# Kernel tuning notes

Hardware: AMD Instinct MI355X
Metric: run time of the kernel (lower is better)

The kernel has to match this reference:

```python
import jax, jax.numpy as jnp
import numpy as np

RU, RV = 6, 6
DU, DV = 2 * RU + 1, 2 * RV + 1  # 13, 13 displacement offsets
C = 32  # feat_channels (WipModule.c_feat)


def _conv(x, w, stride=1, pad=1):
    return jax.lax.conv_general_dilated(
        x, w, (stride, stride), [(pad, pad), (pad, pad)],
        dimension_numbers=('NCHW', 'OIHW', 'NCHW'))


def _deconv(x, w):
    # expressed as an lhs-dilated conv (kernel stored directly in OIHW conv layout).
    p = 4 - 1 - 1
    return jax.lax.conv_general_dilated(
        x, w, (1, 1), [(p, p), (p, p)], lhs_dilation=(2, 2),
        dimension_numbers=('NCHW', 'OIHW', 'NCHW'))


def _kaiming(key, shape):
    fan_in = shape[1] * shape[2] * shape[3]
    return jax.random.normal(key, shape, jnp.float32) * np.float32(np.sqrt(2.0 / fan_in))


def setup_inputs() -> dict:
    key = jax.random.key(0)
    ks = jax.random.split(key, 8)
    B, H, W = 1, 64, 128
    return {
        'fmap1': jax.random.normal(ks[0], (B, C, H, W), jnp.float32),
        'fmap2': jax.random.normal(ks[1], (B, C, H, W), jnp.float32),
        'w1': _kaiming(ks[2], (96, 2 * C, 3, 3)),
        'w2': _kaiming(ks[3], (128, 96, 3, 3)),
        'w3': _kaiming(ks[4], (128, 128, 3, 3)),
        'w4': _kaiming(ks[5], (64, 128, 3, 3)),
        'wd': _kaiming(ks[6], (32, 64, 4, 4)),
        'w5': _kaiming(ks[7], (1, 32, 3, 3)),
    }


def _build_mvol(fmap1, fmap2):
    # Vectorized form of the torch itertools.product loop: one padded gather
    # over all (du, dv) displacement windows instead of 169 slice-assignments.
    b, c, h, w = fmap1.shape
    padded = jnp.pad(fmap2, ((0, 0), (0, 0), (RV, RV), (RU, RU)))

    def window(i, j):
        # shifted(y, x) = fmap2[y + (j - RV), x + (i - RU)], zero outside bounds
        return jax.lax.dynamic_slice(padded, (0, 0, j, i), (b, c, h, w))

    shifted = jax.vmap(lambda i: jax.vmap(lambda j: window(i, j))(jnp.arange(DV)))(jnp.arange(DU))
    shifted = jnp.moveaxis(shifted, 2, 0)  # (b, du, dv, c, h, w)
    # valid mask: detached channel-sum of the warped fmap2 slice (matches torch)
    valid = (jax.lax.stop_gradient(shifted).sum(axis=3, keepdims=True) != 0)
    valid = valid.astype(fmap1.dtype)
    m1 = fmap1[:, None, None] * valid  # broadcast fmap1 over (du, dv)
    return jnp.concatenate([m1, shifted * valid], axis=3)  # (b, du, dv, 2c, h, w)


def reference(fmap1, fmap2, w1, w2, w3, w4, wd, w5):
    mvol = _build_mvol(fmap1, fmap2)
    b, du, dv, c2, h, w = mvol.shape
    # MatchingNet: fold (du, dv) into batch, conv stack down to 1 cost channel
    x = mvol.reshape(b * du * dv, c2, h, w)
    x = jax.nn.relu(_conv(x, w1))
    x = jax.nn.relu(_conv(x, w2, stride=2))  # (.., 128, h/2, w/2)
    x = jax.nn.relu(_conv(x, w3))
    x = jax.nn.relu(_conv(x, w4))
    x = jax.nn.relu(_deconv(x, wd))          # back to (h, w)
    x = _conv(x, w5)                          # cost, 1 channel
    return x.reshape(b, du, dv, h, w)
```

## Files before the change

### kernel.cpp

```cpp
#include <hip/hip_runtime.h>

#define NITEMS 169

typedef __attribute__((ext_vector_type(8))) __bf16 bf16x8;
typedef __attribute__((ext_vector_type(4))) float f32x4;
typedef __attribute__((ext_vector_type(8))) unsigned short u16x8;
typedef __attribute__((ext_vector_type(4))) unsigned short u16x4;

__device__ __forceinline__ unsigned short f2b(float x) {
  union { float f; unsigned u; } v; v.f = x;
  unsigned r = v.u + 0x7fffu + ((v.u >> 16) & 1u);
  return (unsigned short)(r >> 16);
}
__device__ __forceinline__ float b2f(unsigned short u) {
  union { unsigned u; float f; } v; v.u = ((unsigned)u) << 16;
  return v.f;
}

__global__ __launch_bounds__(256) void k_prepf(const float* __restrict__ f,
                                               unsigned short* __restrict__ fb) {
  const int pix = blockIdx.x * 256 + threadIdx.x;
  const int y = pix >> 7, x = pix & 127;
#pragma unroll
  for (int c = 0; c < 32; ++c)
    fb[(size_t)pix * 32 + c] = f2b(f[(c * 64 + y) * 128 + x]);
}

__global__ void k_prep3x3(const float* __restrict__ w, unsigned short* __restrict__ wp,
                          int Cout, int Cin) {
  int i = blockIdx.x * 256 + threadIdx.x;
  if (i >= Cout * Cin * 9) return;
  int kx = i % 3, t = i / 3;
  int ky = t % 3; t /= 3;
  int cin = t % Cin, cout = t / Cin;
  int tap = ky * 3 + kx;
  wp[(((cin >> 5) * 9 + tap) * Cout + cout) * 32 + (cin & 31)] = f2b(w[i]);
}

__global__ void k_prepwd(const float* __restrict__ w, unsigned short* __restrict__ wp) {
  int i = blockIdx.x * 256 + threadIdx.x;
  if (i >= 32 * 64 * 16) return;
  int kx = i & 3, ky = (i >> 2) & 3, ci = (i >> 4) & 63, cout = i >> 10;
  wp[(((((ci >> 5) * 4 + ky) * 4 + kx) * 32) + cout) * 32 + (ci & 31)] = f2b(w[i]);
}

__global__ __launch_bounds__(256) void k_z1(
    const unsigned short* __restrict__ f1b, const unsigned short* __restrict__ wp,
    float* __restrict__ z1) {
  const int oy0 = blockIdx.x * 2;
  constexpr int WI = 130;
  __shared__ __align__(16) unsigned short X[4][4][WI][8];
  const int wid = threadIdx.x >> 6, lane = threadIdx.x & 63;
  const int lm = lane & 15, lkg = lane >> 4, lk = lkg * 8;

  f32x4 acc[24];
#pragma unroll
  for (int t = 0; t < 24; ++t) acc[t] = f32x4{0.f, 0.f, 0.f, 0.f};

  for (int c = threadIdx.x; c < 4 * 4 * WI; c += 256) {
    const int cig = c & 3, t2 = c >> 2;
    const int col = t2 % WI, r = t2 / WI;
    const int iy = oy0 - 1 + r, ix = col - 1;
    u16x8 v = {0, 0, 0, 0, 0, 0, 0, 0};
    if ((unsigned)iy < 64u && (unsigned)ix < 128u)
      v = *(const u16x8*)&f1b[(size_t)(iy * 128 + ix) * 32 + cig * 8];
    *(u16x8*)&X[r][cig][col][0] = v;
  }
  __syncthreads();
#pragma unroll
  for (int tap = 0; tap < 9; ++tap) {
    const int ky = tap / 3, kx = tap % 3;
    bf16x8 bf[4];
#pragma unroll
    for (int j = 0; j < 4; ++j) {
      const int mt = wid * 4 + j, rw = mt >> 3, mtx = mt & 7;
      bf[j] = *(const bf16x8*)&X[rw + ky][lkg][mtx * 16 + lm + kx][0];
    }
#pragma unroll
    for (int i = 0; i < 6; ++i) {
      bf16x8 af = *(const bf16x8*)&wp[((0 * 9 + tap) * 96 + i * 16 + lm) * 32 + lk];
#pragma unroll
      for (int j = 0; j < 4; ++j)
        acc[i * 4 + j] =
            __builtin_amdgcn_mfma_f32_16x16x32_bf16(af, bf[j], acc[i * 4 + j], 0, 0, 0);
    }
  }
#pragma unroll
  for (int i = 0; i < 6; ++i)
#pragma unroll
    for (int j = 0; j < 4; ++j) {
      const int mt = wid * 4 + j, rw = mt >> 3, mtx = mt & 7;
      const int cout0 = i * 16 + lkg * 4;
      const int m = mtx * 16 + lm;
      *(f32x4*)&z1[(size_t)((oy0 + rw) * 128 + m) * 96 + cout0] = acc[i * 4 + j];
    }
}

__global__ __launch_bounds__(256) void k_z2e(
    const unsigned short* __restrict__ f2b_, const unsigned short* __restrict__ wp,
    float* __restrict__ z2e) {
  const int u = blockIdx.x;
  constexpr int WI = 194;
  __shared__ __align__(16) unsigned short X[3][4][WI][8];
  const int wid = threadIdx.x >> 6, lane = threadIdx.x & 63;
  const int lm = lane & 15, lkg = lane >> 4, lk = lkg * 8;

  f32x4 acc[18];
#pragma unroll
  for (int t = 0; t < 18; ++t) acc[t] = f32x4{0.f, 0.f, 0.f, 0.f};

  for (int c = threadIdx.x; c < 3 * 4 * WI; c += 256) {
    const int cig = c & 3, t2 = c >> 2;
    const int col = t2 % WI, r = t2 / WI;
    const int iy = u + r - 7, ix = col - 7;
    u16x8 v = {0, 0, 0, 0, 0, 0, 0, 0};
    if ((unsigned)iy < 64u && (unsigned)ix < 128u)
      v = *(const u16x8*)&f2b_[(size_t)(iy * 128 + ix) * 32 + cig * 8];
    *(u16x8*)&X[r][cig][col][0] = v;
  }
  __syncthreads();
#pragma unroll
  for (int tap = 0; tap < 9; ++tap) {
    const int ky = tap / 3, kx = tap % 3;
    bf16x8 bf[3];
#pragma unroll
    for (int j = 0; j < 3; ++j) {
      const int mt = wid * 3 + j;
      bf[j] = *(const bf16x8*)&X[ky][lkg][mt * 16 + lm + kx][0];
    }
#pragma unroll
    for (int i = 0; i < 6; ++i) {
      bf16x8 af = *(const bf16x8*)&wp[((1 * 9 + tap) * 96 + i * 16 + lm) * 32 + lk];
#pragma unroll
      for (int j = 0; j < 3; ++j)
        acc[i * 3 + j] =
            __builtin_amdgcn_mfma_f32_16x16x32_bf16(af, bf[j], acc[i * 3 + j], 0, 0, 0);
    }
  }
#pragma unroll
  for (int i = 0; i < 6; ++i)
#pragma unroll
    for (int j = 0; j < 3; ++j) {
      const int v = (wid * 3 + j) * 16 + lm;
      if (v < 140) {
        const int cout0 = i * 16 + lkg * 4;
        *(f32x4*)&z2e[(size_t)(u * 140 + v) * 96 + cout0] = acc[i * 3 + j];
      }
    }
}

__global__ __launch_bounds__(256) void k_crow(
    const unsigned short* __restrict__ f1b, const unsigned short* __restrict__ wp,
    float* __restrict__ crow) {
  const int dyi = blockIdx.x / 7, r = blockIdx.x % 7;
  const int dy = dyi - 6;
  const int ady = dy < 0 ? -dy : dy;
  if (dy == 0 || r >= ady + 1) return;
  const int rowlo = dy > 0 ? 63 - dy : 0;
  const int oy = rowlo + r;
  constexpr int WI = 130;
  __shared__ __align__(16) unsigned short X[3][4][WI][8];
  const int wid = threadIdx.x >> 6, lane = threadIdx.x & 63;
  const int lm = lane & 15, lkg = lane >> 4, lk = lkg * 8;

  f32x4 acc[12];
#pragma unroll
  for (int t = 0; t < 12; ++t) acc[t] = f32x4{0.f, 0.f, 0.f, 0.f};

  for (int c = threadIdx.x; c < 3 * 4 * WI; c += 256) {
    const int cig = c & 3, t2 = c >> 2;
    const int col = t2 % WI, rr = t2 / WI;
    const int iy = oy - 1 + rr, ix = col - 1;
    const bool band = dy > 0 ? (iy >= 64 - dy) : (iy < -dy);
    u16x8 v = {0, 0, 0, 0, 0, 0, 0, 0};
    if (band && (unsigned)iy < 64u && (unsigned)ix < 128u)
      v = *(const u16x8*)&f1b[(size_t)(iy * 128 + ix) * 32 + cig * 8];
    *(u16x8*)&X[rr][cig][col][0] = v;
  }
  __syncthreads();
#pragma unroll
  for (int tap = 0; tap < 9; ++tap) {
    const int ky = tap / 3, kx = tap % 3;
    bf16x8 bf[2];
#pragma unroll
    for (int j = 0; j < 2; ++j)
      bf[j] = *(const bf16x8*)&X[ky][lkg][(wid * 2 + j) * 16 + lm + kx][0];
#pragma unroll
    for (int i = 0; i < 6; ++i) {
      bf16x8 af = *(const bf16x8*)&wp[((0 * 9 + tap) * 96 + i * 16 + lm) * 32 + lk];
#pragma unroll
      for (int j = 0; j < 2; ++j)
        acc[i * 2 + j] =
            __builtin_amdgcn_mfma_f32_16x16x32_bf16(af, bf[j], acc[i * 2 + j], 0, 0, 0);
    }
  }
#pragma unroll
  for (int i = 0; i < 6; ++i)
#pragma unroll
    for (int j = 0; j < 2; ++j) {
      const int cout0 = i * 16 + lkg * 4;
      const int m = (wid * 2 + j) * 16 + lm;
      *(f32x4*)&crow[(size_t)((dyi * 8 + r) * 128 + m) * 96 + cout0] = acc[i * 2 + j];
    }
}

__global__ __launch_bounds__(256) void k_ccol(
    const unsigned short* __restrict__ f1b, const unsigned short* __restrict__ wp,
    float* __restrict__ ccol) {
  const int dxi = blockIdx.x;
  const int dx = dxi - 6;
  const int adx = dx < 0 ? -dx : dx;
  if (dx == 0) return;
  const int ccnt = adx + 1;
  const int collo = dx > 0 ? 127 - dx : 0;
  __shared__ __align__(16) unsigned short X2[9][66][32];
  const int wid = threadIdx.x >> 6, lane = threadIdx.x & 63;
  const int lm = lane & 15, lkg = lane >> 4, lk = lkg * 8;

  for (int t = threadIdx.x; t < 9 * 66 * 4; t += 256) {
    const int cig = t & 3, pos = t >> 2;
    const int rr = pos % 66, cc = pos / 66;
    const int iy = rr - 1, ix = collo - 1 + cc;
    const bool band = dx > 0 ? (ix >= 128 - dx) : (ix < -dx);
    u16x8 v = {0, 0, 0, 0, 0, 0, 0, 0};
    if (band && (unsigned)iy < 64u && (unsigned)ix < 128u)
      v = *(const u16x8*)&f1b[(size_t)(iy * 128 + ix) * 32 + cig * 8];
    *(u16x8*)&X2[cc][rr][cig * 8] = v;
  }
  __syncthreads();
  for (int c = 0; c < ccnt; ++c) {
    f32x4 acc[6];
#pragma unroll
    for (int i = 0; i < 6; ++i) acc[i] = f32x4{0.f, 0.f, 0.f, 0.f};
#pragma unroll
    for (int tap = 0; tap < 9; ++tap) {
      const int ky = tap / 3, kx = tap % 3;
      bf16x8 bf = *(const bf16x8*)&X2[c + kx][wid * 16 + lm + ky][lk];
#pragma unroll
      for (int i = 0; i < 6; ++i) {
        bf16x8 af = *(const bf16x8*)&wp[((0 * 9 + tap) * 96 + i * 16 + lm) * 32 + lk];
        acc[i] = __builtin_amdgcn_mfma_f32_16x16x32_bf16(af, bf, acc[i], 0, 0, 0);
      }
    }
    const int y = wid * 16 + lm;
#pragma unroll
    for (int i = 0; i < 6; ++i) {
      const int cout0 = i * 16 + lkg * 4;
      *(f32x4*)&ccol[(size_t)((dxi * 64 + y) * 8 + c) * 96 + cout0] = acc[i];
    }
  }
}

__device__ __forceinline__ float dot32(const unsigned short* __restrict__ xv,
                                       const unsigned short* __restrict__ wv) {
  float s = 0.f;
#pragma unroll
  for (int cg = 0; cg < 4; ++cg) {
    u16x8 a = *(const u16x8*)&xv[cg * 8];
    u16x8 b = *(const u16x8*)&wv[cg * 8];
#pragma unroll
    for (int e = 0; e < 8; ++e) s += b2f(a[e]) * b2f(b[e]);
  }
  return s;
}

__global__ __launch_bounds__(256) void k_ccorner(
    const unsigned short* __restrict__ f1b, const unsigned short* __restrict__ w1p,
    float* __restrict__ ccor) {
  const int idx = blockIdx.x * 256 + threadIdx.x;
  if (idx >= NITEMS * 64 * 96) return;
  const int co = idx % 96, t = idx / 96;
  const int c = t & 7, r = (t >> 3) & 7, item = t >> 6;
  const int dx = item / 13 - 6, dy = item % 13 - 6;
  if (dx == 0 || dy == 0) return;
  const int ady = dy < 0 ? -dy : dy, adx = dx < 0 ? -dx : dx;
  if (r >= ady + 1 || c >= adx + 1) return;
  const int rowlo = dy > 0 ? 63 - dy : 0;
  const int collo = dx > 0 ? 127 - dx : 0;
  const int oy = rowlo + r, ox = collo + c;
  float acc = 0.f;
#pragma unroll
  for (int ky = 0; ky < 3; ++ky)
#pragma unroll
    for (int kx = 0; kx < 3; ++kx) {
      const int iy = oy - 1 + ky, ix = ox - 1 + kx;
      const bool rb = dy > 0 ? (iy >= 64 - dy) : (iy < -dy);
      const bool cb = dx > 0 ? (ix >= 128 - dx) : (ix < -dx);
      if (rb && cb && (unsigned)iy < 64u && (unsigned)ix < 128u)
        acc += dot32(&f1b[(size_t)(iy * 128 + ix) * 32],
                     &w1p[((ky * 3 + kx) * 96 + co) * 32]);
    }
  ccor[(size_t)(((item * 8 + r) * 8 + c) * 96) + co] = acc;
}

__global__ __launch_bounds__(256) void k_bcorr_rows(
    const unsigned short* __restrict__ f2bp, const unsigned short* __restrict__ w1p,
    float* __restrict__ rtop, float* __restrict__ rbot) {
  const int idx = blockIdx.x * 256 + threadIdx.x;
  if (idx >= 13 * 140 * 96) return;
  const int co = idx % 96, t = idx / 96;
  const int v = t % 140, dyi = t / 140;
  const int dy = dyi - 6;
  const int rt = dy - 1, rb = 64 + dy;
  float at = 0.f, ab = 0.f;
#pragma unroll
  for (int kx = 0; kx < 3; ++kx) {
    const int x2 = v - 7 + kx;
    if ((unsigned)x2 >= 128u) continue;
    if ((unsigned)rt < 64u)
      at += dot32(&f2bp[(size_t)(rt * 128 + x2) * 32],
                  &w1p[((9 + 0 + kx) * 96 + co) * 32]);
    if ((unsigned)rb < 64u)
      ab += dot32(&f2bp[(size_t)(rb * 128 + x2) * 32],
                  &w1p[((9 + 6 + kx) * 96 + co) * 32]);
  }
  rtop[idx] = at;
  rbot[idx] = ab;
}

__global__ __launch_bounds__(256) void k_bcorr_cols(
    const unsigned short* __restrict__ f2bp, const unsigned short* __restrict__ w1p,
    float* __restrict__ clft, float* __restrict__ crgt) {
  const int idx = blockIdx.x * 256 + threadIdx.x;
  if (idx >= 13 * 76 * 96) return;
  const int co = idx % 96, t = idx / 96;
  const int u = t % 76, dxi = t / 76;
  const int dx = dxi - 6;
  const int cl = dx - 1, cr = 128 + dx;
  float al = 0.f, ar = 0.f;
#pragma unroll
  for (int ky = 0; ky < 3; ++ky) {
    const int y2 = u - 7 + ky;
    if ((unsigned)y2 >= 64u) continue;
    if ((unsigned)cl < 128u)
      al += dot32(&f2bp[(size_t)(y2 * 128 + cl) * 32],
                  &w1p[((9 + ky * 3 + 0) * 96 + co) * 32]);
    if ((unsigned)cr < 128u)
      ar += dot32(&f2bp[(size_t)(y2 * 128 + cr) * 32],
                  &w1p[((9 + ky * 3 + 2) * 96 + co) * 32]);
  }
  clft[idx] = al;
  crgt[idx] = ar;
}

__global__ __launch_bounds__(256) void k_bcorr_corn(
    const unsigned short* __restrict__ f2bp, const unsigned short* __restrict__ w1p,
    float* __restrict__ kcorn) {
  const int idx = blockIdx.x * 256 + threadIdx.x;
  if (idx >= NITEMS * 4 * 96) return;
  const int co = idx % 96, t = idx / 96;
  const int corner = t % 4, item = t / 4;
  const int dx = item / 13 - 6, dy = item % 13 - 6;
  const int row = (corner < 2) ? dy - 1 : 64 + dy;
  const int col = (corner & 1) ? 128 + dx : dx - 1;
  const int ky = (corner < 2) ? 0 : 2;
  const int kx = (corner & 1) ? 2 : 0;
  float acc = 0.f;
  if ((unsigned)row < 64u && (unsigned)col < 128u)
    acc = dot32(&f2bp[(size_t)(row * 128 + col) * 32],
                &w1p[((9 + ky * 3 + kx) * 96 + co) * 32]);
  kcorn[idx] = acc;
}

struct ItemGeo {
  int item, dx, dy, dyi, dxi, rowlo, rowhi, collo, colhi;
};

__device__ __forceinline__ u16x8 x1_fuse8(
    const float* __restrict__ z1, const float* __restrict__ z2e,
    const float* __restrict__ crow, const float* __restrict__ ccol,
    const float* __restrict__ ccor, const float* __restrict__ rtop,
    const float* __restrict__ rbot, const float* __restrict__ clft,
    const float* __restrict__ crgt, const float* __restrict__ kcorn,
    const ItemGeo& gm, int y, int px, int c0) {
  const bool inrow = (y >= gm.rowlo) && (y < gm.rowhi);
  const bool incol = (px >= gm.collo) && (px < gm.colhi);
  const int vrow = y + gm.dy + 6;
  const int v = px + gm.dx + 6;
  u16x8 o;
#pragma unroll
  for (int h = 0; h < 2; ++h) {
    const int cc = c0 + h * 4;
    f32x4 s = *(const f32x4*)&z1[(size_t)(y * 128 + px) * 96 + cc];
    s += *(const f32x4*)&z2e[(size_t)(vrow * 140 + v) * 96 + cc];
    if (inrow)
      s -= *(const f32x4*)&crow[(size_t)((gm.dyi * 8 + y - gm.rowlo) * 128 + px) * 96 + cc];
    if (incol) {
      s -= *(const f32x4*)&ccol[(size_t)((gm.dxi * 64 + y) * 8 + px - gm.collo) * 96 + cc];
      if (inrow)
        s += *(const f32x4*)&ccor[(size_t)(((gm.item * 8 + y - gm.rowlo) * 8) + px - gm.collo) * 96 + cc];
    }
    if (y == 0) s -= *(const f32x4*)&rtop[(size_t)(gm.dyi * 140 + v) * 96 + cc];
    if (y == 63) s -= *(const f32x4*)&rbot[(size_t)(gm.dyi * 140 + v) * 96 + cc];
    if (px == 0) s -= *(const f32x4*)&clft[(size_t)(gm.dxi * 76 + vrow) * 96 + cc];
    if (px == 127) s -= *(const f32x4*)&crgt[(size_t)(gm.dxi * 76 + vrow) * 96 + cc];
    if (y == 0 && px == 0) s += *(const f32x4*)&kcorn[(size_t)gm.item * 384 + 0 * 96 + cc];
    if (y == 0 && px == 127) s += *(const f32x4*)&kcorn[(size_t)gm.item * 384 + 1 * 96 + cc];
    if (y == 63 && px == 0) s += *(const f32x4*)&kcorn[(size_t)gm.item * 384 + 2 * 96 + cc];
    if (y == 63 && px == 127) s += *(const f32x4*)&kcorn[(size_t)gm.item * 384 + 3 * 96 + cc];
#pragma unroll
    for (int e = 0; e < 4; ++e) o[h * 4 + e] = f2b(fmaxf(s[e], 0.f));
  }
  return o;
}

__global__ __launch_bounds__(256) void k_conv2f(
    const float* __restrict__ z1, const float* __restrict__ z2e,
    const float* __restrict__ crow, const float* __restrict__ ccol,
    const float* __restrict__ ccor, const float* __restrict__ rtop,
    const float* __restrict__ rbot, const float* __restrict__ clft,
    const float* __restrict__ crgt, const float* __restrict__ kcorn,
    const unsigned short* __restrict__ wp, unsigned short* __restrict__ x2,
    int base) {
  constexpr int WI = 130, WIH = 65;
  const int g = blockIdx.y, oy = blockIdx.x;
  const int item = base + g;
  ItemGeo gm;
  gm.item = item;
  gm.dx = item / 13 - 6;
  gm.dy = item % 13 - 6;
  gm.dyi = gm.dy + 6;
  gm.dxi = gm.dx + 6;
  {
    const int ady = gm.dy < 0 ? -gm.dy : gm.dy, adx = gm.dx < 0 ? -gm.dx : gm.dx;
    gm.rowlo = gm.dy > 0 ? 63 - gm.dy : 0;
    gm.rowhi = gm.rowlo + (gm.dy ? ady + 1 : 0);
    gm.collo = gm.dx > 0 ? 127 - gm.dx : 0;
    gm.colhi = gm.collo + (gm.dx ? adx + 1 : 0);
  }
  unsigned short* op = x2 + (size_t)g * (128 * 2048);
  __shared__ __align__(16) unsigned short X[3][4][WI][8];
  const int wid = threadIdx.x >> 6, lane = threadIdx.x & 63;
  const int lm = lane & 15, lkg = lane >> 4, lk = lkg * 8;
  const int ct0 = wid * 2;

  f32x4 acc[8];
#pragma unroll
  for (int t = 0; t < 8; ++t) acc[t] = f32x4{0.f, 0.f, 0.f, 0.f};

  for (int cic = 0; cic < 3; ++cic) {
    __syncthreads();
    for (int c = threadIdx.x; c < 3 * 4 * WI; c += 256) {
      const int cig = c & 3, t2 = c >> 2;
      const int col = t2 % WI, r = t2 / WI;
      const int iy = oy * 2 - 1 + r, ix = col - 1;
      const int pcol = (col >> 1) + (col & 1) * WIH;
      u16x8 v = {0, 0, 0, 0, 0, 0, 0, 0};
      if ((unsigned)iy < 64u && (unsigned)ix < 128u)
        v = x1_fuse8(z1, z2e, crow, ccol, ccor, rtop, rbot, clft, crgt, kcorn,
                     gm, iy, ix, cic * 32 + cig * 8);
      *(u16x8*)&X[r][cig][pcol][0] = v;
    }
    __syncthreads();
#pragma unroll
    for (int tap = 0; tap < 9; ++tap) {
      const int ky = tap / 3, kx = tap % 3;
      bf16x8 bf[4];
#pragma unroll
      for (int j = 0; j < 4; ++j) {
        const int m = j * 16 + lm;
        const int colr = m + (kx >> 1) + (kx & 1) * WIH;
        bf[j] = *(const bf16x8*)&X[ky][lkg][colr][0];
      }
#pragma unroll
      for (int i = 0; i < 2; ++i) {
        const int cout = (ct0 + i) * 16 + lm;
        bf16x8 af = *(const bf16x8*)&wp[((cic * 9 + tap) * 128 + cout) * 32 + lk];
#pragma unroll
        for (int j = 0; j < 4; ++j)
          acc[i * 4 + j] =
              __builtin_amdgcn_mfma_f32_16x16x32_bf16(af, bf[j], acc[i * 4 + j], 0, 0, 0);
      }
    }
  }
#pragma unroll
  for (int i = 0; i < 2; ++i)
#pragma unroll
    for (int j = 0; j < 4; ++j) {
      const int cout0 = (ct0 + i) * 16 + lkg * 4;
      const int m = j * 16 + lm;
      u16x4 pv;
#pragma unroll
      for (int r = 0; r < 4; ++r) pv[r] = f2b(fmaxf(acc[i * 4 + j][r], 0.f));
      *(u16x4*)&op[(size_t)(oy * 64 + m) * 128 + cout0] = pv;
    }
}

template <int Cin, int Cout, int H, int W, int STRIDE, bool RELU>
__global__ __launch_bounds__(256) void k_convm(
    const unsigned short* __restrict__ xin, const unsigned short* __restrict__ wp,
    unsigned short* __restrict__ xout) {
  constexpr int OH = H / STRIDE, OW = W / STRIDE;
  constexpr int WI = W + 2;
  constexpr int WIH = (WI + 1) / 2;
  constexpr int NC = Cout / 16, NM = OW / 16;
  static_assert(NC % 4 == 0, "cout tiles divisible by 4 waves");
  constexpr int WCT = NC / 4, WMT = NM;
  const int g = blockIdx.y, oy = blockIdx.x;
  const unsigned short* ip = xin + (size_t)g * Cin * H * W;
  unsigned short* op = xout + (size_t)g * Cout * OH * OW;
  __shared__ __align__(16) unsigned short X[3][4][WI][8];
  const int wid = threadIdx.x >> 6, lane = threadIdx.x & 63;
  const int lm = lane & 15, lkg = lane >> 4, lk = lkg * 8;
  const int ct0 = wid * WCT;

  f32x4 acc[WCT * WMT];
#pragma unroll
  for (int t = 0; t < WCT * WMT; ++t) acc[t] = f32x4{0.f, 0.f, 0.f, 0.f};

  for (int cic = 0; cic < Cin / 32; ++cic) {
    __syncthreads();
    for (int c = threadIdx.x; c < 3 * 4 * WI; c += 256) {
      const int cig = c & 3, t2 = c >> 2;
      const int col = t2 % WI, r = t2 / WI;
      const int iy = oy * STRIDE - 1 + r, ix = col - 1;
      const int pcol = (STRIDE == 2) ? ((col >> 1) + (col & 1) * WIH) : col;
      u16x8 v = {0, 0, 0, 0, 0, 0, 0, 0};
      if ((unsigned)iy < (unsigned)H && (unsigned)ix < (unsigned)W)
        v = *(const u16x8*)&ip[(size_t)(iy * W + ix) * Cin + cic * 32 + cig * 8];
      *(u16x8*)&X[r][cig][pcol][0] = v;
    }
    __syncthreads();
#pragma unroll
    for (int tap = 0; tap < 9; ++tap) {
      const int ky = tap / 3, kx = tap % 3;
      bf16x8 bf[WMT];
#pragma unroll
      for (int j = 0; j < WMT; ++j) {
        const int m = j * 16 + lm;
        const int colr = (STRIDE == 2) ? (m + (kx >> 1) + (kx & 1) * WIH) : (m + kx);
        bf[j] = *(const bf16x8*)&X[ky][lkg][colr][0];
      }
#pragma unroll
      for (int i = 0; i < WCT; ++i) {
        const int cout = (ct0 + i) * 16 + lm;
        bf16x8 af = *(const bf16x8*)&wp[((cic * 9 + tap) * Cout + cout) * 32 + lk];
#pragma unroll
        for (int j = 0; j < WMT; ++j)
          acc[i * WMT + j] =
              __builtin_amdgcn_mfma_f32_16x16x32_bf16(af, bf[j], acc[i * WMT + j], 0, 0, 0);
      }
    }
  }
#pragma unroll
  for (int i = 0; i < WCT; ++i)
#pragma unroll
    for (int j = 0; j < WMT; ++j) {
      const int cout0 = (ct0 + i) * 16 + lkg * 4;
      const int m = j * 16 + lm;
      u16x4 pv;
#pragma unroll
      for (int r = 0; r < 4; ++r) {
        float f = acc[i * WMT + j][r];
        if (RELU) f = fmaxf(f, 0.f);
        pv[r] = f2b(f);
      }
      *(u16x4*)&op[(size_t)(oy * OW + m) * Cout + cout0] = pv;
    }
}

__global__ __launch_bounds__(256) void k_deconvm(
    const unsigned short* __restrict__ x4, const unsigned short* __restrict__ wp,
    unsigned short* __restrict__ x5) {
  const int g = blockIdx.y, mrow = blockIdx.x;
  const unsigned short* ip = x4 + (size_t)g * (2048 * 64);
  unsigned short* op = x5 + (size_t)g * (8192 * 32);
  constexpr int WI = 66;
  __shared__ __align__(16) unsigned short X[3][4][WI][8];
  const int wid = threadIdx.x >> 6, lane = threadIdx.x & 63;
  const int a = wid >> 1, b = wid & 1;
  const int lm = lane & 15, lkg = lane >> 4, lk = lkg * 8;
  f32x4 acc[8];
#pragma unroll
  for (int t = 0; t < 8; ++t) acc[t] = f32x4{0.f, 0.f, 0.f, 0.f};

  for (int cic = 0; cic < 2; ++cic) {
    __syncthreads();
    for (int c = threadIdx.x; c < 3 * 4 * WI; c += 256) {
      const int cig = c & 3, t2 = c >> 2;
      const int col = t2 % WI, r = t2 / WI;
      const int iy = mrow - 1 + r, ix = col - 1;
      u16x8 v = {0, 0, 0, 0, 0, 0, 0, 0};
      if ((unsigned)iy < 32u && (unsigned)ix < 64u)
        v = *(const u16x8*)&ip[(size_t)(iy * 64 + ix) * 64 + cic * 32 + cig * 8];
      *(u16x8*)&X[r][cig][col][0] = v;
    }
    __syncthreads();
#pragma unroll
    for (int u = 0; u < 2; ++u)
#pragma unroll
      for (int vv = 0; vv < 2; ++vv) {
        const int r = (a == 0) ? u : u + 1;
        const int ky = (a == 0) ? 2 * u : 2 * u + 1;
        const int s = (b == 0) ? vv : vv + 1;
        const int kx = (b == 0) ? 2 * vv : 2 * vv + 1;
        bf16x8 bf[4];
#pragma unroll
        for (int j = 0; j < 4; ++j)
          bf[j] = *(const bf16x8*)&X[r][lkg][j * 16 + lm + s][0];
#pragma unroll
        for (int i = 0; i < 2; ++i) {
          bf16x8 af =
              *(const bf16x8*)&wp[((((cic * 4 + ky) * 4 + kx) * 32) + i * 16 + lm) * 32 + lk];
#pragma unroll
          for (int j = 0; j < 4; ++j)
            acc[i * 4 + j] =
                __builtin_amdgcn_mfma_f32_16x16x32_bf16(af, bf[j], acc[i * 4 + j], 0, 0, 0);
        }
      }
  }
#pragma unroll
  for (int i = 0; i < 2; ++i)
#pragma unroll
    for (int j = 0; j < 4; ++j) {
      const int cout0 = i * 16 + lkg * 4;
      const int p = j * 16 + lm;
      const int orow = 2 * mrow + a, ocol = 2 * p + b;
      u16x4 pv;
#pragma unroll
      for (int r2 = 0; r2 < 4; ++r2) pv[r2] = f2b(fmaxf(acc[i * 4 + j][r2], 0.f));
      *(u16x4*)&op[(size_t)(orow * 128 + ocol) * 32 + cout0] = pv;
    }
}

__global__ __launch_bounds__(256) void k_conv5m(
    const unsigned short* __restrict__ x5, const float* __restrict__ w5,
    float* __restrict__ out) {
  const int g = blockIdx.y;
  const int pix = blockIdx.x * 256 + threadIdx.x;
  const int y = pix >> 7, x = pix & 127;
  const unsigned short* ip = x5 + (size_t)g * (8192 * 32);
  float s = 0.f;
#pragma unroll
  for (int t = 0; t < 9; ++t) {
    const int yy = y - 1 + t / 3, xx = x - 1 + t % 3;
    if ((unsigned)yy < 64u && (unsigned)xx < 128u) {
#pragma unroll
      for (int cg = 0; cg < 4; ++cg) {
        u16x8 v = *(const u16x8*)&ip[(size_t)(yy * 128 + xx) * 32 + cg * 8];
#pragma unroll
        for (int e = 0; e < 8; ++e) s += b2f(v[e]) * w5[(cg * 8 + e) * 9 + t];
      }
    }
  }
  out[(size_t)g * 8192 + pix] = s;
}

extern "C" void kernel_launch(void* const* d_in, const int* in_sizes, int n_in,
                              void* d_out, int out_size, void* d_ws, size_t ws_size,
                              hipStream_t stream) {
  const float* f1 = (const float*)d_in[0];
  const float* f2 = (const float*)d_in[1];
  const float* w1 = (const float*)d_in[2];
  const float* w2 = (const float*)d_in[3];
  const float* w3 = (const float*)d_in[4];
  const float* w4 = (const float*)d_in[5];
  const float* wd = (const float*)d_in[6];
  const float* w5 = (const float*)d_in[7];
  float* out = (float*)d_out;

  size_t off = 0;
  auto alloc = [&](size_t bytes) {
    void* p = (char*)d_ws + off;
    off += (bytes + 255) / 256 * 256;
    return p;
  };
  unsigned short* f1b = (unsigned short*)alloc(64 * 128 * 32 * 2);
  unsigned short* f2bp = (unsigned short*)alloc(64 * 128 * 32 * 2);
  unsigned short* w1p = (unsigned short*)alloc(2 * 9 * 96 * 32 * 2);
  unsigned short* w2p = (unsigned short*)alloc(3 * 9 * 128 * 32 * 2);
  unsigned short* w3p = (unsigned short*)alloc(4 * 9 * 128 * 32 * 2);
  unsigned short* w4p = (unsigned short*)alloc(4 * 9 * 64 * 32 * 2);
  unsigned short* wdp = (unsigned short*)alloc(2 * 16 * 32 * 32 * 2);
  float* z1 = (float*)alloc((size_t)64 * 128 * 96 * 4);
  float* z2e = (float*)alloc((size_t)76 * 140 * 96 * 4);
  float* crow = (float*)alloc((size_t)13 * 8 * 128 * 96 * 4);
  float* ccol = (float*)alloc((size_t)13 * 64 * 8 * 96 * 4);
  float* ccor = (float*)alloc((size_t)NITEMS * 8 * 8 * 96 * 4);
  float* rtop = (float*)alloc((size_t)13 * 140 * 96 * 4);
  float* rbot = (float*)alloc((size_t)13 * 140 * 96 * 4);
  float* clft = (float*)alloc((size_t)13 * 76 * 96 * 4);
  float* crgt = (float*)alloc((size_t)13 * 76 * 96 * 4);
  float* kcorn = (float*)alloc((size_t)NITEMS * 4 * 96 * 4);
  const size_t wend = off;

  const size_t perSlot = (size_t)128 * 2048 * 2;
  int G = (int)((ws_size - wend) / (2 * perSlot));
  if (G > NITEMS) G = NITEMS;
  if (G < 1) G = 1;
  unsigned short* P = (unsigned short*)((char*)d_ws + wend);
  unsigned short* Q = (unsigned short*)((char*)d_ws + wend + (size_t)G * perSlot);

  k_prepf<<<32, 256, 0, stream>>>(f1, f1b);
  k_prepf<<<32, 256, 0, stream>>>(f2, f2bp);
  k_prep3x3<<<(96 * 64 * 9 + 255) / 256, 256, 0, stream>>>(w1, w1p, 96, 64);
  k_prep3x3<<<(128 * 96 * 9 + 255) / 256, 256, 0, stream>>>(w2, w2p, 128, 96);
  k_prep3x3<<<(128 * 128 * 9 + 255) / 256, 256, 0, stream>>>(w3, w3p, 128, 128);
  k_prep3x3<<<(64 * 128 * 9 + 255) / 256, 256, 0, stream>>>(w4, w4p, 64, 128);
  k_prepwd<<<(32 * 64 * 16 + 255) / 256, 256, 0, stream>>>(wd, wdp);

  k_z1<<<32, 256, 0, stream>>>(f1b, w1p, z1);
  k_z2e<<<76, 256, 0, stream>>>(f2bp, w1p, z2e);
  k_crow<<<91, 256, 0, stream>>>(f1b, w1p, crow);
  k_ccol<<<13, 256, 0, stream>>>(f1b, w1p, ccol);
  k_ccorner<<<(NITEMS * 64 * 96 + 255) / 256, 256, 0, stream>>>(f1b, w1p, ccor);
  k_bcorr_rows<<<(13 * 140 * 96 + 255) / 256, 256, 0, stream>>>(f2bp, w1p, rtop, rbot);
  k_bcorr_cols<<<(13 * 76 * 96 + 255) / 256, 256, 0, stream>>>(f2bp, w1p, clft, crgt);
  k_bcorr_corn<<<(NITEMS * 4 * 96 + 255) / 256, 256, 0, stream>>>(f2bp, w1p, kcorn);

  for (int base = 0; base < NITEMS; base += G) {
    const int cnt = (NITEMS - base < G) ? (NITEMS - base) : G;
    k_conv2f<<<dim3(32, cnt), 256, 0, stream>>>(z1, z2e, crow, ccol, ccor, rtop, rbot,
                                                clft, crgt, kcorn, w2p, P, base);
    k_convm<128, 128, 32, 64, 1, true><<<dim3(32, cnt), 256, 0, stream>>>(P, w3p, Q);
    k_convm<128, 64, 32, 64, 1, true><<<dim3(32, cnt), 256, 0, stream>>>(Q, w4p, P);
    k_deconvm<<<dim3(32, cnt), 256, 0, stream>>>(P, wdp, Q);
    k_conv5m<<<dim3(32, cnt), 256, 0, stream>>>(Q, w5, out + (size_t)base * 8192);
  }
}
```

Before: 702.9 us.

## Split conv2 input staging into fast interior path and boundary fixup passes

The staging loop of the fused conv2 kernel previously ran the full boundary-aware x1_fuse8 routine for every pixel. Now interior pixels take a cheap path: load z1 and the shifted z2e, add, ReLU, and convert to bf16 with the hardware cast. Boundary columns, edge rows and the valid-mask transition rows are then overwritten in two extra passes using the exact routine. This cuts per-pixel ALU and gather work but adds two barriers and some redundant writes, and it relies on the fixup passes covering every pixel where the cheap formula is wrong.

```diff
diff --git a/kernel.cpp b/kernel.cpp
--- a/kernel.cpp
+++ b/kernel.cpp
@@ -11,6 +11,11 @@
   union { float f; unsigned u; } v; v.f = x;
   unsigned r = v.u + 0x7fffu + ((v.u >> 16) & 1u);
   return (unsigned short)(r >> 16);
+}
+__device__ __forceinline__ unsigned short f2b2(float x) {
+  __bf16 b = (__bf16)x;
+  union { __bf16 b; unsigned short u; } v; v.b = b;
+  return v.u;
 }
 __device__ __forceinline__ float b2f(unsigned short u) {
   union { unsigned u; float f; } v; v.u = ((unsigned)u) << 16;
@@ -421,13 +426,19 @@
   gm.dy = item % 13 - 6;
   gm.dyi = gm.dy + 6;
   gm.dxi = gm.dx + 6;
-  {
-    const int ady = gm.dy < 0 ? -gm.dy : gm.dy, adx = gm.dx < 0 ? -gm.dx : gm.dx;
-    gm.rowlo = gm.dy > 0 ? 63 - gm.dy : 0;
-    gm.rowhi = gm.rowlo + (gm.dy ? ady + 1 : 0);
-    gm.collo = gm.dx > 0 ? 127 - gm.dx : 0;
-    gm.colhi = gm.collo + (gm.dx ? adx + 1 : 0);
-  }
+  const int ady = gm.dy < 0 ? -gm.dy : gm.dy, adx = gm.dx < 0 ? -gm.dx : gm.dx;
+  gm.rowlo = gm.dy > 0 ? 63 - gm.dy : 0;
+  gm.rowhi = gm.rowlo + (gm.dy ? ady + 1 : 0);
+  gm.collo = gm.dx > 0 ? 127 - gm.dx : 0;
+  gm.colhi = gm.collo + (gm.dx ? adx + 1 : 0);
+
+  bool anyrow = false;
+#pragma unroll
+  for (int r = 0; r < 3; ++r) {
+    const int iy = oy * 2 - 1 + r;
+    anyrow |= ((iy >= gm.rowlo && iy < gm.rowhi) || iy == 0 || iy == 63);
+  }
+
   unsigned short* op = x2 + (size_t)g * (128 * 2048);
   __shared__ __align__(16) unsigned short X[3][4][WI][8];
   const int wid = threadIdx.x >> 6, lane = threadIdx.x & 63;
@@ -446,10 +457,55 @@
       const int iy = oy * 2 - 1 + r, ix = col - 1;
       const int pcol = (col >> 1) + (col & 1) * WIH;
       u16x8 v = {0, 0, 0, 0, 0, 0, 0, 0};
-      if ((unsigned)iy < 64u && (unsigned)ix < 128u)
-        v = x1_fuse8(z1, z2e, crow, ccol, ccor, rtop, rbot, clft, crgt, kcorn,
-                     gm, iy, ix, cic * 32 + cig * 8);
+      if ((unsigned)iy < 64u && (unsigned)ix < 128u) {
+        const float* p1 = &z1[(size_t)(iy * 128 + ix) * 96 + cic * 32 + cig * 8];
+        const float* p2 =
+            &z2e[(size_t)((iy + gm.dy + 6) * 140 + (ix + gm.dx + 6)) * 96 + cic * 32 + cig * 8];
+        f32x4 a0 = *(const f32x4*)p1;
+        f32x4 a1 = *(const f32x4*)(p1 + 4);
+        f32x4 b0 = *(const f32x4*)p2;
+        f32x4 b1 = *(const f32x4*)(p2 + 4);
+        f32x4 s0 = a0 + b0, s1 = a1 + b1;
+#pragma unroll
+        for (int e = 0; e < 4; ++e) v[e] = f2b2(fmaxf(s0[e], 0.f));
+#pragma unroll
+        for (int e = 0; e < 4; ++e) v[4 + e] = f2b2(fmaxf(s1[e], 0.f));
+      }
       *(u16x8*)&X[r][cig][pcol][0] = v;
+    }
+    __syncthreads();
+    for (int e = threadIdx.x; e < 3 * 9 * 4; e += 256) {
+      const int cig = e & 3, t2 = e >> 2;
+      const int k = t2 % 9, r = t2 / 9;
+      int px;
+      if (k < 7) {
+        if (gm.dx == 0 || k > adx) continue;
+        px = gm.collo + k;
+      } else {
+        px = (k == 7) ? 0 : 127;
+      }
+      const int iy = oy * 2 - 1 + r;
+      if ((unsigned)iy >= 64u) continue;
+      u16x8 v = x1_fuse8(z1, z2e, crow, ccol, ccor, rtop, rbot, clft, crgt, kcorn,
+                         gm, iy, px, cic * 32 + cig * 8);
+      const int col = px + 1;
+      const int pcol = (col >> 1) + (col & 1) * WIH;
+      *(u16x8*)&X[r][cig][pcol][0] = v;
+    }
+    __syncthreads();
+    if (anyrow) {
+      for (int c = threadIdx.x; c < 3 * 4 * WI; c += 256) {
+        const int cig = c & 3, t2 = c >> 2;
+        const int col = t2 % WI, r = t2 / WI;
+        const int iy = oy * 2 - 1 + r, ix = col - 1;
+        const bool rn = ((iy >= gm.rowlo && iy < gm.rowhi) || iy == 0 || iy == 63);
+        if (!rn || (unsigned)iy >= 64u || (unsigned)ix >= 128u) continue;
+        u16x8 v = x1_fuse8(z1, z2e, crow, ccol, ccor, rtop, rbot, clft, crgt, kcorn,
+                           gm, iy, ix, cic * 32 + cig * 8);
+        const int pcol = (col >> 1) + (col & 1) * WIH;
+        *(u16x8*)&X[r][cig][pcol][0] = v;
+      }
+      __syncthreads();
     }
     __syncthreads();
 #pragma unroll
```

Result: slower. 787.4 us (+12.0%).
